# Kernel tuning notes

Hardware: AMD Instinct MI355X
Metric: run time of the kernel (lower is better)

Reference implementation:

```python
import jax, jax.numpy as jnp
import numpy as np

B, C, T = 8, 512, 4096          # batch, channels (query/key/value/calc), time
NUM_HEADS = 8
HEAD_DIM = C // NUM_HEADS
EPS = 1e-6


def _rmsnorm(x, g):
    # x: [B, C, T], normalize over channel dim (num_features)
    return x * jax.lax.rsqrt(jnp.mean(x * x, axis=1, keepdims=True) + EPS) * g[None, :, None]


def _conv1x1(x, W, b):
    # pointwise Conv1d: W [out, in], x [B, in, T]
    return jnp.einsum('oc,bct->bot', W, x) + b[None, :, None]


def _feature(x, W, b, g):
    # Conv1d -> RMSNorm -> elu(x)+1
    return jax.nn.elu(_rmsnorm(_conv1x1(x, W, b), g)) + 1.0


def setup_inputs() -> dict:
    key = jax.random.key(0)
    ks = jax.random.split(key, 16)
    s = 1.0 / np.sqrt(C)
    inp = {
        'queries': jax.random.normal(ks[0], (B, C, T), dtype=jnp.float32),
        'keys': jax.random.normal(ks[1], (B, C, T), dtype=jnp.float32),
        'values': jax.random.normal(ks[2], (B, C, T), dtype=jnp.float32),
        'key_padding_masks': jax.random.randint(ks[3], (B, T), 0, 2).astype(bool),
        'Wq': jax.random.normal(ks[4], (C, C), dtype=jnp.float32) * s,
        'bq': jnp.zeros((C,), dtype=jnp.float32),
        'gq': jnp.ones((C,), dtype=jnp.float32),
        'Wk': jax.random.normal(ks[5], (C, C), dtype=jnp.float32) * s,
        'bk': jnp.zeros((C,), dtype=jnp.float32),
        'gk': jnp.ones((C,), dtype=jnp.float32),
        'Wv': jax.random.normal(ks[6], (C, C), dtype=jnp.float32) * s,
        'bv': jnp.zeros((C,), dtype=jnp.float32),
        'gv': jnp.ones((C,), dtype=jnp.float32),
        'Wp': jax.random.normal(ks[7], (C, C), dtype=jnp.float32) * s,
        'bp': jnp.zeros((C,), dtype=jnp.float32),
        'g_out': jnp.ones((C,), dtype=jnp.float32),
    }
    return inp


def reference(queries, keys, values, key_padding_masks,
              Wq, bq, gq, Wk, bk, gk, Wv, bv, gv, Wp, bp, g_out):
    residuals = queries
    q = _feature(queries, Wq, bq, gq)   # [B, C, Tq]
    k = _feature(keys, Wk, bk, gk)      # [B, C, Tk]
    v = _feature(values, Wv, bv, gv)    # [B, C, Tk]

    # split heads: (head dim) channel layout -> [B, H, Dh, T]
    q = q.reshape(B, NUM_HEADS, HEAD_DIM, -1)
    k = k.reshape(B, NUM_HEADS, HEAD_DIM, -1)
    v = v.reshape(B, NUM_HEADS, HEAD_DIM, -1)

    k = jnp.where(key_padding_masks[:, None, None, :], -10000.0, k)

    q = jax.nn.softmax(q, axis=2) * (NUM_HEADS ** -0.5)  # softmax over head_dim
    k = jax.nn.softmax(k, axis=3)                         # softmax over key time
    v = v / HEAD_DIM

    # linear attention: KV composition then QKV
    ctx = jnp.einsum('bhkt,bhvt->bhkv', k, v)             # [B, H, Dh, Dh]
    out = jnp.einsum('bhqt,bhqv->bhvt', q, ctx)           # [B, H, Dh, Tq]

    out = out.reshape(B, C, -1)
    out = _conv1x1(out, Wp, bp)
    return _rmsnorm(out + residuals, g_out)
```

## Files before the change

kernel.cpp:

```cpp
#include <hip/hip_runtime.h>
#include <hip/hip_bf16.h>

#define BB 8
#define CC 512
#define TT 4096
#define HH 8
#define DH 64
#define EPS 1e-6f

#define NROWS (BB * TT)

using bf16x8 = __attribute__((ext_vector_type(8))) short;
using s16x4  = __attribute__((ext_vector_type(4))) short;
using f32x4  = __attribute__((ext_vector_type(4))) float;

__device__ __forceinline__ short f2b(float f) {
  __hip_bfloat16 h = __float2bfloat16(f);
  return *reinterpret_cast<short*>(&h);
}
__device__ __forceinline__ float b2f(short s) {
  unsigned u = ((unsigned)(unsigned short)s) << 16;
  return __uint_as_float(u);
}

__device__ __forceinline__ void gld16(short* lds_dst, const short* gsrc) {
  __builtin_amdgcn_global_load_lds(
      (const __attribute__((address_space(1))) unsigned int*)gsrc,
      (__attribute__((address_space(3))) unsigned int*)lds_dst, 16, 0, 0);
}

__global__ __launch_bounds__(256) void conv_w4(const float* __restrict__ s0, const float* __restrict__ s1,
                                               const float* __restrict__ s2, const float* __restrict__ s3,
                                               short* __restrict__ d0, short* __restrict__ d1,
                                               short* __restrict__ d2, short* __restrict__ d3)
{
  const float* src; short* dst;
  switch (blockIdx.y) {
    case 0: src = s0; dst = d0; break;
    case 1: src = s1; dst = d1; break;
    case 2: src = s2; dst = d2; break;
    default: src = s3; dst = d3; break;
  }
  int i8 = (blockIdx.x * 256 + threadIdx.x) * 8;
  float4 a = *(const float4*)(src + i8);
  float4 b = *(const float4*)(src + i8 + 4);
  bf16x8 h = { f2b(a.x), f2b(a.y), f2b(a.z), f2b(a.w),
               f2b(b.x), f2b(b.y), f2b(b.z), f2b(b.w) };
  *(bf16x8*)(dst + i8) = h;
}

#define TSTR 120
__device__ __forceinline__ int tadr(int c, int t) {
  return c * TSTR + ((c >> 3) & 7) * 8 + t;
}

__global__ __launch_bounds__(256) void transpose_cvt3(const float* __restrict__ X0,
                                                      const float* __restrict__ X1,
                                                      const float* __restrict__ X2,
                                                      short* __restrict__ Y0,
                                                      short* __restrict__ Y1,
                                                      short* __restrict__ Y2)
{
  __shared__ short tile[2][64 * TSTR];
  const int t0 = blockIdx.x * 256, c0 = blockIdx.y * 64;
  const int b = blockIdx.z & 7, which = blockIdx.z >> 3;
  const float* X = which == 0 ? X0 : (which == 1 ? X1 : X2);
  short* Xt = which == 0 ? Y0 : (which == 1 ? Y1 : Y2);
  const int tid = threadIdx.x;
  const int cl = tid >> 4, t4 = (tid & 15) * 4;
  const int T2 = (tid >> 3) * 2, ci = (tid & 7) * 8;

  float4 r[4];
  #pragma unroll
  for (int it = 0; it < 4; ++it)
    r[it] = *(const float4*)(X + ((size_t)b * CC + c0 + it * 16 + cl) * TT + t0 + t4);

  for (int s = 0; s < 4; ++s) {
    const int cur = s & 1;
    #pragma unroll
    for (int it = 0; it < 4; ++it) {
      s16x4 h = { f2b(r[it].x), f2b(r[it].y), f2b(r[it].z), f2b(r[it].w) };
      *(s16x4*)&tile[cur][tadr(it * 16 + cl, t4)] = h;
    }
    if (s < 3) {
      #pragma unroll
      for (int it = 0; it < 4; ++it)
        r[it] = *(const float4*)(X + ((size_t)b * CC + c0 + it * 16 + cl) * TT
                                 + t0 + (s + 1) * 64 + t4);
    }
    __syncthreads();
    unsigned u[8];
    #pragma unroll
    for (int i = 0; i < 8; ++i)
      u[i] = *(const unsigned*)&tile[cur][tadr(ci + i, T2)];
    short lo[8], hi[8];
    #pragma unroll
    for (int i = 0; i < 8; ++i) {
      lo[i] = (short)(u[i] & 0xffffu);
      hi[i] = (short)(u[i] >> 16);
    }
    short* dst0 = Xt + ((size_t)b * TT + t0 + s * 64 + T2) * CC + c0 + ci;
    *(bf16x8*)dst0 = *(bf16x8*)&lo[0];
    *(bf16x8*)(dst0 + CC) = *(bf16x8*)&hi[0];
  }
}

__device__ __forceinline__ void gemm_body(const short* __restrict__ A,
                                          const short* __restrict__ W,
                                          const float* __restrict__ bias,
                                          short* __restrict__ Y,
                                          short* As, short* Bs, int x, int tid)
{
  int wg = (x & 7) * 128 + (x >> 3);
  const int m0 = (wg >> 2) * 128;
  const int o0 = (wg & 3) * 128;

  const int wid = tid >> 6, lane = tid & 63;
  const int wr = (wid >> 1) * 64, wc = (wid & 1) * 64;
  const int lr = lane & 15, g = lane >> 4;
  const int swz8 = (g ^ ((lr >> 1) & 3)) * 8;

  const int srow0 = tid >> 2;
  const int scol  = ((tid & 3) ^ ((tid >> 3) & 3)) * 8;

  f32x4 acc[4][4] = {};

  #pragma unroll
  for (int it = 0; it < 2; ++it) {
    int row = it * 64 + srow0;
    gld16(&As[it * 2048 + tid * 8], A + (size_t)(m0 + row) * CC + scol);
    gld16(&Bs[it * 2048 + tid * 8], W + (size_t)(o0 + row) * CC + scol);
  }
  __syncthreads();

  for (int step = 0; step < 16; ++step) {
    const int cur = step & 1;
    if (step < 15) {
      const int k0 = (step + 1) * 32;
      #pragma unroll
      for (int it = 0; it < 2; ++it) {
        int row = it * 64 + srow0;
        gld16(&As[(cur ^ 1) * 4096 + it * 2048 + tid * 8], A + (size_t)(m0 + row) * CC + k0 + scol);
        gld16(&Bs[(cur ^ 1) * 4096 + it * 2048 + tid * 8], W + (size_t)(o0 + row) * CC + k0 + scol);
      }
    }
    bf16x8 af[4], bf[4];
    #pragma unroll
    for (int m = 0; m < 4; ++m) af[m] = *(const bf16x8*)&As[cur * 4096 + (wr + m * 16 + lr) * 32 + swz8];
    #pragma unroll
    for (int n = 0; n < 4; ++n) bf[n] = *(const bf16x8*)&Bs[cur * 4096 + (wc + n * 16 + lr) * 32 + swz8];
    #pragma unroll
    for (int m = 0; m < 4; ++m)
      #pragma unroll
      for (int n = 0; n < 4; ++n)
        acc[m][n] = __builtin_amdgcn_mfma_f32_16x16x32_bf16(af[m], bf[n], acc[m][n], 0, 0, 0);
    __syncthreads();
  }

  const int lq4 = (lane >> 4) * 4;
  #pragma unroll
  for (int m = 0; m < 4; ++m)
    #pragma unroll
    for (int r = 0; r < 4; ++r) {
      size_t row = (size_t)(m0 + wr + m * 16 + lq4 + r) * CC;
      #pragma unroll
      for (int n = 0; n < 4; ++n) {
        int o = o0 + wc + n * 16 + lr;
        Y[row + o] = f2b(acc[m][n][r] + bias[o]);
      }
    }
}

__global__ __launch_bounds__(256) void gemm_tc3(
    const short* __restrict__ A0, const short* __restrict__ A1, const short* __restrict__ A2,
    const short* __restrict__ W0, const short* __restrict__ W1, const short* __restrict__ W2,
    const float* __restrict__ b0, const float* __restrict__ b1, const float* __restrict__ b2,
    short* __restrict__ Y0, short* __restrict__ Y1, short* __restrict__ Y2)
{
  __shared__ short As[2 * 4096];
  __shared__ short Bs[2 * 4096];
  const short *A, *W; const float* bias; short* Y;
  switch (blockIdx.y) {
    case 0:  A = A0; W = W0; bias = b0; Y = Y0; break;
    case 1:  A = A1; W = W1; bias = b1; Y = Y1; break;
    default: A = A2; W = W2; bias = b2; Y = Y2; break;
  }
  gemm_body(A, W, bias, Y, As, Bs, blockIdx.x, threadIdx.x);
}

__global__ __launch_bounds__(256) void gemm_tc(const short* __restrict__ A,
                                               const short* __restrict__ W,
                                               const float* __restrict__ bias,
                                               short* __restrict__ Y)
{
  __shared__ short As[2 * 4096];
  __shared__ short Bs[2 * 4096];
  gemm_body(A, W, bias, Y, As, Bs, blockIdx.x, threadIdx.x);
}

__global__ __launch_bounds__(256) void feat_all(short* __restrict__ qf, short* __restrict__ kf,
                                                short* __restrict__ vf,
                                                const float* __restrict__ gq,
                                                const float* __restrict__ gk,
                                                const float* __restrict__ gv,
                                                const unsigned char* __restrict__ mask)
{
  const int mode = blockIdx.y;
  short* buf = mode == 0 ? qf : (mode == 1 ? kf : vf);
  const float* g = mode == 0 ? gq : (mode == 1 ? gk : gv);
  const int row = blockIdx.x * 4 + (threadIdx.x >> 6);
  const int lane = threadIdx.x & 63;
  short* p = buf + (size_t)row * CC + lane * 8;
  if (mode == 1 && mask[row]) {
    bf16x8 z = { 0,0,0,0,0,0,0,0 };
    *(bf16x8*)p = z;
    return;
  }
  bf16x8 v = *(const bf16x8*)p;
  float x[8], ss = 0.f;
  #pragma unroll
  for (int j = 0; j < 8; ++j) { x[j] = b2f(v[j]); ss += x[j] * x[j]; }
  #pragma unroll
  for (int off = 32; off; off >>= 1) ss += __shfl_xor(ss, off);
  float rn = rsqrtf(ss * (1.0f / CC) + EPS);
  float4 g0 = *(const float4*)(g + lane * 8);
  float4 g1 = *(const float4*)(g + lane * 8 + 4);
  float gv8[8] = { g0.x, g0.y, g0.z, g0.w, g1.x, g1.y, g1.z, g1.w };
  float f[8];
  #pragma unroll
  for (int j = 0; j < 8; ++j) {
    float t = x[j] * rn * gv8[j];
    f[j] = t > 0.f ? t + 1.f : __expf(t);
  }
  bf16x8 o;
  if (mode == 1) {
    #pragma unroll
    for (int j = 0; j < 8; ++j) o[j] = f2b(__expf(f[j]));
  } else if (mode == 2) {
    #pragma unroll
    for (int j = 0; j < 8; ++j) o[j] = f2b(f[j] * (1.0f / DH));
  } else {
    float ls = 0.f;
    #pragma unroll
    for (int j = 0; j < 8; ++j) { f[j] = __expf(f[j]); ls += f[j]; }
    ls += __shfl_xor(ls, 1); ls += __shfl_xor(ls, 2); ls += __shfl_xor(ls, 4);
    float sc = 0.35355339059327373f / ls;
    #pragma unroll
    for (int j = 0; j < 8; ++j) o[j] = f2b(f[j] * sc);
  }
  *(bf16x8*)p = o;
}

__global__ __launch_bounds__(256) void ksm_sum(const short* __restrict__ kfe,
                                               float* __restrict__ S)
{
  const int b = blockIdx.y, tch = blockIdx.x;
  const int c2 = threadIdx.x * 2;
  float s0 = 0.f, s1 = 0.f;
  for (int t = 0; t < 128; ++t) {
    unsigned u = *(const unsigned*)&kfe[((size_t)b * TT + tch * 128 + t) * CC + c2];
    s0 += __uint_as_float(u << 16);
    s1 += __uint_as_float(u & 0xffff0000u);
  }
  atomicAdd(&S[b * CC + c2], s0);
  atomicAdd(&S[b * CC + c2 + 1], s1);
}

__global__ __launch_bounds__(256) void ctx_t(const short* __restrict__ kf,
                                             const short* __restrict__ vf,
                                             float* __restrict__ P)
{
  __shared__ short Ks[64 * 64];
  __shared__ short Vs[64 * 64];
  const int tc = blockIdx.x, bh = blockIdx.y;
  const int b = bh >> 3, h = bh & 7;
  const int tid = threadIdx.x, wid = tid >> 6, lane = tid & 63;
  const int lr = lane & 15, lg = lane >> 4;
  f32x4 acc[4] = {};

  for (int ts = 0; ts < 8; ++ts) {
    #pragma unroll
    for (int i = 0; i < 2; ++i) {
      int n = i * 256 + tid;
      int t = n >> 3, ch = (n & 7) * 8;
      size_t src = ((size_t)b * TT + tc * 512 + ts * 64 + t) * CC + h * DH + ch;
      gld16(Ks + n * 8, kf + src);
      gld16(Vs + n * 8, vf + src);
    }
    __syncthreads();
    #pragma unroll
    for (int kk = 0; kk < 64; kk += 32) {
      short a[8];
      #pragma unroll
      for (int j = 0; j < 8; ++j)
        a[j] = Ks[(kk + lg * 8 + j) * 64 + wid * 16 + lr];
      bf16x8 af = *(const bf16x8*)&a[0];
      #pragma unroll
      for (int n = 0; n < 4; ++n) {
        short bv[8];
        #pragma unroll
        for (int j = 0; j < 8; ++j)
          bv[j] = Vs[(kk + lg * 8 + j) * 64 + n * 16 + lr];
        acc[n] = __builtin_amdgcn_mfma_f32_16x16x32_bf16(af, *(const bf16x8*)&bv[0],
                                                         acc[n], 0, 0, 0);
      }
    }
    __syncthreads();
  }
  float* pp = P + ((size_t)tc * 64 + bh) * (DH * DH);
  const int lq4 = lg * 4;
  #pragma unroll
  for (int n = 0; n < 4; ++n)
    #pragma unroll
    for (int r = 0; r < 4; ++r)
      pp[(wid * 16 + lq4 + r) * DH + n * 16 + lr] = acc[n][r];
}

__global__ __launch_bounds__(256) void ctx_reduce(const float* __restrict__ P,
                                                  const float* __restrict__ S,
                                                  short* __restrict__ CT)
{
  int i = blockIdx.x * 256 + threadIdx.x;
  float s = 0.f;
  #pragma unroll
  for (int c = 0; c < 8; ++c) s += P[(size_t)c * 64 * DH * DH + i];
  int bh = i >> 12, rem = i & 4095, q = rem >> 6, v = rem & 63;
  int b = bh >> 3, h = bh & 7;
  float inv = 1.f / S[b * CC + h * DH + q];
  CT[((size_t)bh << 12) + v * 64 + q] = f2b(s * inv);
}

__global__ __launch_bounds__(256) void attn_t(const short* __restrict__ qf,
                                              const short* __restrict__ CT,
                                              short* __restrict__ ao)
{
  __shared__ short As[128 * 72];
  __shared__ short Cs[64 * 72];
  const int m0 = blockIdx.x * 128, h = blockIdx.y;
  const int tid = threadIdx.x, wid = tid >> 6, lane = tid & 63;
  const int lr = lane & 15, lk8 = (lane >> 4) * 8;

  #pragma unroll
  for (int i = 0; i < 4; ++i) {
    int n = i * 256 + tid;
    int r = n >> 3, ch = (n & 7) * 8;
    *(bf16x8*)&As[r * 72 + ch] =
        *(const bf16x8*)(qf + (size_t)(m0 + r) * CC + h * DH + ch);
  }
  {
    const int bh0 = (m0 / TT) * 8 + h;
    #pragma unroll
    for (int i = 0; i < 2; ++i) {
      int n = i * 256 + tid;
      int v = n >> 3, ch = (n & 7) * 8;
      *(bf16x8*)&Cs[v * 72 + ch] = *(const bf16x8*)(CT + ((size_t)bh0 << 12) + v * 64 + ch);
    }
  }
  __syncthreads();

  const int wr = wid * 32;
  f32x4 acc[2][4] = {};
  #pragma unroll
  for (int kk = 0; kk < 64; kk += 32) {
    bf16x8 af[2], cf[4];
    #pragma unroll
    for (int m = 0; m < 2; ++m) af[m] = *(const bf16x8*)&As[(wr + m * 16 + lr) * 72 + kk + lk8];
    #pragma unroll
    for (int n = 0; n < 4; ++n) cf[n] = *(const bf16x8*)&Cs[(n * 16 + lr) * 72 + kk + lk8];
    #pragma unroll
    for (int m = 0; m < 2; ++m)
      #pragma unroll
      for (int n = 0; n < 4; ++n)
        acc[m][n] = __builtin_amdgcn_mfma_f32_16x16x32_bf16(af[m], cf[n], acc[m][n], 0, 0, 0);
  }
  const int lq4 = (lane >> 4) * 4;
  #pragma unroll
  for (int m = 0; m < 2; ++m)
    #pragma unroll
    for (int r = 0; r < 4; ++r) {
      size_t row = (size_t)(m0 + wr + m * 16 + lq4 + r) * CC + h * DH;
      #pragma unroll
      for (int n = 0; n < 4; ++n)
        ao[row + n * 16 + lr] = f2b(acc[m][n][r]);
    }
}

__global__ __launch_bounds__(256) void final_fused(const short* __restrict__ pj,
                                                   const short* __restrict__ qt,
                                                   const float* __restrict__ g,
                                                   float* __restrict__ out)
{
  __shared__ short z[512 * 72];
  __shared__ float rmss[64];
  const int t0 = blockIdx.x * 64, b = blockIdx.y;
  const int tid = threadIdx.x;

  {
    const int t = tid >> 2, cb = (tid & 3) * 128;
    const size_t row = ((size_t)b * TT + t0 + t) * CC + cb;
    float ss = 0.f;
    #pragma unroll
    for (int j = 0; j < 16; ++j) {
      bf16x8 a = *(const bf16x8*)(pj + row + j * 8);
      bf16x8 q = *(const bf16x8*)(qt + row + j * 8);
      #pragma unroll
      for (int e = 0; e < 8; ++e) {
        float zf = b2f(a[e]) + b2f(q[e]);
        ss += zf * zf;
        z[(cb + j * 8 + e) * 72 + t] = f2b(zf);
      }
    }
    ss += __shfl_xor(ss, 1);
    ss += __shfl_xor(ss, 2);
    if ((tid & 3) == 0) rmss[t] = rsqrtf(ss * (1.0f / CC) + EPS);
  }
  __syncthreads();

  const int c = tid >> 2, tcs = (tid & 3) * 16;
  #pragma unroll 1
  for (int cb8 = 0; cb8 < 8; ++cb8) {
    const int cc = cb8 * 64 + c;
    const float gc = g[cc];
    bf16x8 z0 = *(const bf16x8*)&z[cc * 72 + tcs];
    bf16x8 z1 = *(const bf16x8*)&z[cc * 72 + tcs + 8];
    float* dst = out + ((size_t)b * CC + cc) * TT + t0 + tcs;
    #pragma unroll
    for (int i = 0; i < 2; ++i) {
      float4 o0 = { b2f(z0[i*4+0]) * rmss[tcs+i*4+0] * gc, b2f(z0[i*4+1]) * rmss[tcs+i*4+1] * gc,
                    b2f(z0[i*4+2]) * rmss[tcs+i*4+2] * gc, b2f(z0[i*4+3]) * rmss[tcs+i*4+3] * gc };
      *(float4*)(dst + i * 4) = o0;
    }
    #pragma unroll
    for (int i = 0; i < 2; ++i) {
      float4 o1 = { b2f(z1[i*4+0]) * rmss[tcs+8+i*4+0] * gc, b2f(z1[i*4+1]) * rmss[tcs+8+i*4+1] * gc,
                    b2f(z1[i*4+2]) * rmss[tcs+8+i*4+2] * gc, b2f(z1[i*4+3]) * rmss[tcs+8+i*4+3] * gc };
      *(float4*)(dst + 8 + i * 4) = o1;
    }
  }
}

extern "C" void kernel_launch(void* const* d_in, const int* in_sizes, int n_in,
                              void* d_out, int out_size, void* d_ws, size_t ws_size,
                              hipStream_t stream) {
  (void)in_sizes; (void)n_in; (void)out_size; (void)ws_size;
  const float* queries = (const float*)d_in[0];
  const float* keys    = (const float*)d_in[1];
  const float* values  = (const float*)d_in[2];
  const unsigned char* mask = (const unsigned char*)d_in[3];
  const float* Wq = (const float*)d_in[4];
  const float* bq = (const float*)d_in[5];
  const float* gq = (const float*)d_in[6];
  const float* Wk = (const float*)d_in[7];
  const float* bk = (const float*)d_in[8];
  const float* gk = (const float*)d_in[9];
  const float* Wv = (const float*)d_in[10];
  const float* bv = (const float*)d_in[11];
  const float* gv = (const float*)d_in[12];
  const float* Wp = (const float*)d_in[13];
  const float* bp = (const float*)d_in[14];
  const float* g_out = (const float*)d_in[15];

  const size_t NCT = (size_t)NROWS * CC;
  short* qt = (short*)d_ws;
  short* kt = qt + NCT;
  short* vt = kt + NCT;
  short* qf = vt + NCT;
  short* kf = qf + NCT;
  short* vf = kf + NCT;
  short* ao = kt;
  short* pj = vt;
  float* ctxP = (float*)(vf + NCT);
  short* CT  = (short*)(ctxP + (size_t)8 * 64 * DH * DH);
  short* wqb = CT + (size_t)64 * DH * DH;
  short* wkb = wqb + (size_t)CC * CC;
  short* wvb = wkb + (size_t)CC * CC;
  short* wpb = wvb + (size_t)CC * CC;
  float* S   = (float*)(wpb + (size_t)CC * CC);

  hipMemsetAsync(S, 0, (size_t)BB * CC * sizeof(float), stream);

  conv_w4<<<dim3(CC * CC / 2048, 4), 256, 0, stream>>>(Wq, Wk, Wv, Wp, wqb, wkb, wvb, wpb);

  transpose_cvt3<<<dim3(TT / 256, CC / 64, 3 * BB), 256, 0, stream>>>(
      queries, keys, values, qt, kt, vt);

  gemm_tc3<<<dim3(1024, 3), 256, 0, stream>>>(qt, kt, vt, wqb, wkb, wvb,
                                              bq, bk, bv, qf, kf, vf);

  feat_all<<<dim3(NROWS / 4, 3), 256, 0, stream>>>(qf, kf, vf, gq, gk, gv, mask);

  ksm_sum<<<dim3(32, BB), 256, 0, stream>>>(kf, S);

  ctx_t<<<dim3(8, BB * HH), 256, 0, stream>>>(kf, vf, ctxP);
  ctx_reduce<<<dim3(64 * DH * DH / 256), 256, 0, stream>>>(ctxP, S, CT);

  attn_t<<<dim3(NROWS / 128, HH), 256, 0, stream>>>(qf, CT, ao);

  gemm_tc<<<dim3(1024), 256, 0, stream>>>(ao, wpb, bp, pj);

  final_fused<<<dim3(TT / 64, BB), 256, 0, stream>>>(pj, qt, g_out, (float*)d_out);
}
```

Before: 315.4 us.

## Replace syncthreads with fine-grained vmcnt waits and raw barriers in transpose and GEMM

The GEMM main loop now waits with s_waitcnt vmcnt(4) before its barrier, so the next tile's async global-to-LDS loads can stay in flight while the current tile is consumed. Previously __syncthreads drained every outstanding load. The transpose kernel drops its double-buffered LDS tile for a single buffer, prefetches the next chunk into registers before writing the current one, and uses raw s_barrier plus sched_barrier fences. This is meant to cut LDS use and stall time, at the risk of subtle races if the vmcnt counts or barrier placement are wrong.

```diff
diff --git a/kernel.cpp b/kernel.cpp
--- a/kernel.cpp
+++ b/kernel.cpp
@@ -61,7 +61,7 @@
                                                       short* __restrict__ Y1,
                                                       short* __restrict__ Y2)
 {
-  __shared__ short tile[2][64 * TSTR];
+  __shared__ short tile[64 * TSTR];
   const int t0 = blockIdx.x * 256, c0 = blockIdx.y * 64;
   const int b = blockIdx.z & 7, which = blockIdx.z >> 3;
   const float* X = which == 0 ? X0 : (which == 1 ? X1 : X2);
@@ -70,29 +70,32 @@
   const int cl = tid >> 4, t4 = (tid & 15) * 4;
   const int T2 = (tid >> 3) * 2, ci = (tid & 7) * 8;
 
-  float4 r[4];
+  float4 rc[4];
   #pragma unroll
   for (int it = 0; it < 4; ++it)
-    r[it] = *(const float4*)(X + ((size_t)b * CC + c0 + it * 16 + cl) * TT + t0 + t4);
-
+    rc[it] = *(const float4*)(X + ((size_t)b * CC + c0 + it * 16 + cl) * TT + t0 + t4);
+
+  #pragma unroll
   for (int s = 0; s < 4; ++s) {
-    const int cur = s & 1;
+    float4 rn[4];
+    if (s < 3) {
+      #pragma unroll
+      for (int it = 0; it < 4; ++it)
+        rn[it] = *(const float4*)(X + ((size_t)b * CC + c0 + it * 16 + cl) * TT
+                                  + t0 + (s + 1) * 64 + t4);
+    }
     #pragma unroll
     for (int it = 0; it < 4; ++it) {
-      s16x4 h = { f2b(r[it].x), f2b(r[it].y), f2b(r[it].z), f2b(r[it].w) };
-      *(s16x4*)&tile[cur][tadr(it * 16 + cl, t4)] = h;
-    }
-    if (s < 3) {
-      #pragma unroll
-      for (int it = 0; it < 4; ++it)
-        r[it] = *(const float4*)(X + ((size_t)b * CC + c0 + it * 16 + cl) * TT
-                                 + t0 + (s + 1) * 64 + t4);
-    }
-    __syncthreads();
+      s16x4 h = { f2b(rc[it].x), f2b(rc[it].y), f2b(rc[it].z), f2b(rc[it].w) };
+      *(s16x4*)&tile[tadr(it * 16 + cl, t4)] = h;
+    }
+    asm volatile("s_waitcnt lgkmcnt(0)" ::: "memory");
+    __builtin_amdgcn_s_barrier();
+    __builtin_amdgcn_sched_barrier(0);
     unsigned u[8];
     #pragma unroll
     for (int i = 0; i < 8; ++i)
-      u[i] = *(const unsigned*)&tile[cur][tadr(ci + i, T2)];
+      u[i] = *(const unsigned*)&tile[tadr(ci + i, T2)];
     short lo[8], hi[8];
     #pragma unroll
     for (int i = 0; i < 8; ++i) {
@@ -102,6 +105,11 @@
     short* dst0 = Xt + ((size_t)b * TT + t0 + s * 64 + T2) * CC + c0 + ci;
     *(bf16x8*)dst0 = *(bf16x8*)&lo[0];
     *(bf16x8*)(dst0 + CC) = *(bf16x8*)&hi[0];
+    __builtin_amdgcn_sched_barrier(0);
+    __builtin_amdgcn_s_barrier();
+    __builtin_amdgcn_sched_barrier(0);
+    #pragma unroll
+    for (int it = 0; it < 4; ++it) rc[it] = rn[it];
   }
 }
 
@@ -131,7 +139,6 @@
     gld16(&As[it * 2048 + tid * 8], A + (size_t)(m0 + row) * CC + scol);
     gld16(&Bs[it * 2048 + tid * 8], W + (size_t)(o0 + row) * CC + scol);
   }
-  __syncthreads();
 
   for (int step = 0; step < 16; ++step) {
     const int cur = step & 1;
@@ -143,7 +150,13 @@
         gld16(&As[(cur ^ 1) * 4096 + it * 2048 + tid * 8], A + (size_t)(m0 + row) * CC + k0 + scol);
         gld16(&Bs[(cur ^ 1) * 4096 + it * 2048 + tid * 8], W + (size_t)(o0 + row) * CC + k0 + scol);
       }
-    }
+      asm volatile("s_waitcnt vmcnt(4)" ::: "memory");
+    } else {
+      asm volatile("s_waitcnt vmcnt(0)" ::: "memory");
+    }
+    __builtin_amdgcn_s_barrier();
+    __builtin_amdgcn_sched_barrier(0);
+
     bf16x8 af[4], bf[4];
     #pragma unroll
     for (int m = 0; m < 4; ++m) af[m] = *(const bf16x8*)&As[cur * 4096 + (wr + m * 16 + lr) * 32 + swz8];
@@ -154,7 +167,10 @@
       #pragma unroll
       for (int n = 0; n < 4; ++n)
         acc[m][n] = __builtin_amdgcn_mfma_f32_16x16x32_bf16(af[m], bf[n], acc[m][n], 0, 0, 0);
-    __syncthreads();
+
+    __builtin_amdgcn_sched_barrier(0);
+    __builtin_amdgcn_s_barrier();
+    __builtin_amdgcn_sched_barrier(0);
   }
 
   const int lq4 = (lane >> 4) * 4;
```

Result: no change. 320.6 us (+1.7%).

## Fuse per-head attention output with output projection GEMM in one kernel

Applied to the files above, without the earlier changes.

Replaces the separate attn_t kernel and the projection GEMM with a single kernel. For each head, the kernel computes the Q·ctx tile into shared memory and immediately accumulates it against the matching slice of Wp. This removes the round trip of the ao intermediate through global memory and one launch. In exchange, each 128x128 output tile recomputes the Q·ctx product for all 8 heads, so 4 column tiles repeat it, and the loop has per-head syncs and no double buffering.

```diff
diff --git a/kernel.cpp b/kernel.cpp
--- a/kernel.cpp
+++ b/kernel.cpp
@@ -185,16 +185,6 @@
     case 1:  A = A1; W = W1; bias = b1; Y = Y1; break;
     default: A = A2; W = W2; bias = b2; Y = Y2; break;
   }
-  gemm_body(A, W, bias, Y, As, Bs, blockIdx.x, threadIdx.x);
-}
-
-__global__ __launch_bounds__(256) void gemm_tc(const short* __restrict__ A,
-                                               const short* __restrict__ W,
-                                               const float* __restrict__ bias,
-                                               short* __restrict__ Y)
-{
-  __shared__ short As[2 * 4096];
-  __shared__ short Bs[2 * 4096];
   gemm_body(A, W, bias, Y, As, Bs, blockIdx.x, threadIdx.x);
 }
 
@@ -330,58 +320,100 @@
   CT[((size_t)bh << 12) + v * 64 + q] = f2b(s * inv);
 }
 
-__global__ __launch_bounds__(256) void attn_t(const short* __restrict__ qf,
-                                              const short* __restrict__ CT,
-                                              short* __restrict__ ao)
-{
-  __shared__ short As[128 * 72];
+__global__ __launch_bounds__(256) void attn_proj(const short* __restrict__ qf,
+                                                 const short* __restrict__ CT,
+                                                 const short* __restrict__ Wp,
+                                                 const float* __restrict__ bp,
+                                                 short* __restrict__ pj)
+{
+  __shared__ short Qs[128 * 72];
   __shared__ short Cs[64 * 72];
-  const int m0 = blockIdx.x * 128, h = blockIdx.y;
-  const int tid = threadIdx.x, wid = tid >> 6, lane = tid & 63;
-  const int lr = lane & 15, lk8 = (lane >> 4) * 8;
-
-  #pragma unroll
-  for (int i = 0; i < 4; ++i) {
-    int n = i * 256 + tid;
-    int r = n >> 3, ch = (n & 7) * 8;
-    *(bf16x8*)&As[r * 72 + ch] =
-        *(const bf16x8*)(qf + (size_t)(m0 + r) * CC + h * DH + ch);
-  }
-  {
-    const int bh0 = (m0 / TT) * 8 + h;
+  __shared__ short Ws2[128 * 72];
+  __shared__ short AOs[128 * 72];
+  const int tid = threadIdx.x;
+  int x = blockIdx.x;
+  int wg = (x & 7) * 128 + (x >> 3);
+  const int m0 = (wg >> 2) * 128;
+  const int o0 = (wg & 3) * 128;
+  const int wid = tid >> 6, lane = tid & 63;
+  const int lr = lane & 15, lg = lane >> 4, lk8 = lg * 8;
+  const int wr = (wid >> 1) * 64, wc = (wid & 1) * 64;
+  const int bh0 = (m0 >> 12) * 8;
+
+  f32x4 acc[4][4] = {};
+
+  for (int h = 0; h < 8; ++h) {
+    #pragma unroll
+    for (int i = 0; i < 4; ++i) {
+      int n = i * 256 + tid;
+      int r = n >> 3, ch = (n & 7) * 8;
+      *(bf16x8*)&Qs[r * 72 + ch]  = *(const bf16x8*)(qf + (size_t)(m0 + r) * CC + h * DH + ch);
+      *(bf16x8*)&Ws2[r * 72 + ch] = *(const bf16x8*)(Wp + (size_t)(o0 + r) * CC + h * DH + ch);
+    }
     #pragma unroll
     for (int i = 0; i < 2; ++i) {
       int n = i * 256 + tid;
       int v = n >> 3, ch = (n & 7) * 8;
-      *(bf16x8*)&Cs[v * 72 + ch] = *(const bf16x8*)(CT + ((size_t)bh0 << 12) + v * 64 + ch);
-    }
-  }
-  __syncthreads();
-
-  const int wr = wid * 32;
-  f32x4 acc[2][4] = {};
-  #pragma unroll
-  for (int kk = 0; kk < 64; kk += 32) {
-    bf16x8 af[2], cf[4];
-    #pragma unroll
-    for (int m = 0; m < 2; ++m) af[m] = *(const bf16x8*)&As[(wr + m * 16 + lr) * 72 + kk + lk8];
-    #pragma unroll
-    for (int n = 0; n < 4; ++n) cf[n] = *(const bf16x8*)&Cs[(n * 16 + lr) * 72 + kk + lk8];
-    #pragma unroll
-    for (int m = 0; m < 2; ++m)
-      #pragma unroll
-      for (int n = 0; n < 4; ++n)
-        acc[m][n] = __builtin_amdgcn_mfma_f32_16x16x32_bf16(af[m], cf[n], acc[m][n], 0, 0, 0);
-  }
-  const int lq4 = (lane >> 4) * 4;
-  #pragma unroll
-  for (int m = 0; m < 2; ++m)
+      *(bf16x8*)&Cs[v * 72 + ch] = *(const bf16x8*)(CT + ((size_t)(bh0 + h) << 12) + v * 64 + ch);
+    }
+    __syncthreads();
+
+    f32x4 aoacc[2][4] = {};
+    #pragma unroll
+    for (int ks = 0; ks < 2; ++ks) {
+      bf16x8 afq[2], cfv[4];
+      #pragma unroll
+      for (int mf = 0; mf < 2; ++mf)
+        afq[mf] = *(const bf16x8*)&Qs[(wid * 32 + mf * 16 + lr) * 72 + ks * 32 + lk8];
+      #pragma unroll
+      for (int nf = 0; nf < 4; ++nf)
+        cfv[nf] = *(const bf16x8*)&Cs[(nf * 16 + lr) * 72 + ks * 32 + lk8];
+      #pragma unroll
+      for (int mf = 0; mf < 2; ++mf)
+        #pragma unroll
+        for (int nf = 0; nf < 4; ++nf)
+          aoacc[mf][nf] = __builtin_amdgcn_mfma_f32_16x16x32_bf16(afq[mf], cfv[nf], aoacc[mf][nf], 0, 0, 0);
+    }
+    #pragma unroll
+    for (int mf = 0; mf < 2; ++mf)
+      #pragma unroll
+      for (int r = 0; r < 4; ++r) {
+        int row = wid * 32 + mf * 16 + lg * 4 + r;
+        #pragma unroll
+        for (int nf = 0; nf < 4; ++nf)
+          AOs[row * 72 + nf * 16 + lr] = f2b(aoacc[mf][nf][r]);
+      }
+    __syncthreads();
+
+    #pragma unroll
+    for (int ks = 0; ks < 2; ++ks) {
+      bf16x8 afa[4], bfw[4];
+      #pragma unroll
+      for (int mf = 0; mf < 4; ++mf)
+        afa[mf] = *(const bf16x8*)&AOs[(wr + mf * 16 + lr) * 72 + ks * 32 + lk8];
+      #pragma unroll
+      for (int nf = 0; nf < 4; ++nf)
+        bfw[nf] = *(const bf16x8*)&Ws2[(wc + nf * 16 + lr) * 72 + ks * 32 + lk8];
+      #pragma unroll
+      for (int mf = 0; mf < 4; ++mf)
+        #pragma unroll
+        for (int nf = 0; nf < 4; ++nf)
+          acc[mf][nf] = __builtin_amdgcn_mfma_f32_16x16x32_bf16(afa[mf], bfw[nf], acc[mf][nf], 0, 0, 0);
+    }
+    __syncthreads();
+  }
+
+  const int lq4 = lg * 4;
+  #pragma unroll
+  for (int mf = 0; mf < 4; ++mf)
     #pragma unroll
     for (int r = 0; r < 4; ++r) {
-      size_t row = (size_t)(m0 + wr + m * 16 + lq4 + r) * CC + h * DH;
-      #pragma unroll
-      for (int n = 0; n < 4; ++n)
-        ao[row + n * 16 + lr] = f2b(acc[m][n][r]);
+      size_t row = (size_t)(m0 + wr + mf * 16 + lq4 + r) * CC;
+      #pragma unroll
+      for (int nf = 0; nf < 4; ++nf) {
+        int o = o0 + wc + nf * 16 + lr;
+        pj[row + o] = f2b(acc[mf][nf][r] + bp[o]);
+      }
     }
 }
 
@@ -467,7 +499,6 @@
   short* qf = vt + NCT;
   short* kf = qf + NCT;
   short* vf = kf + NCT;
-  short* ao = kt;
   short* pj = vt;
   float* ctxP = (float*)(vf + NCT);
   short* CT  = (short*)(ctxP + (size_t)8 * 64 * DH * DH);
@@ -494,9 +525,7 @@
   ctx_t<<<dim3(8, BB * HH), 256, 0, stream>>>(kf, vf, ctxP);
   ctx_reduce<<<dim3(64 * DH * DH / 256), 256, 0, stream>>>(ctxP, S, CT);
 
-  attn_t<<<dim3(NROWS / 128, HH), 256, 0, stream>>>(qf, CT, ao);
-
-  gemm_tc<<<dim3(1024), 256, 0, stream>>>(ao, wpb, bp, pj);
+  attn_proj<<<dim3(1024), 256, 0, stream>>>(qf, CT, wpb, bp, pj);
 
   final_fused<<<dim3(TT / 64, BB), 256, 0, stream>>>(pj, qt, g_out, (float*)d_out);
 }
```

Result: slower. 323.4 us (+2.5%).

## Fuse fp32-to-bf16 transpose into GEMM for key and value projections

Applied to the files above, without the earlier changes.

Keys and values no longer go through a separate transpose-and-convert pass to bf16 [B*T, C] buffers. A new GEMM kernel reads the fp32 [B, C, T] input directly, converts it to bf16 and transposes it into a swizzled LDS tile while prefetching the next K-slice in registers. Queries still use the old transpose path because the transposed bf16 copy is needed later as the residual. This removes one full write and re-read of two activation tensors, at the cost of fp32 global loads inside the GEMM main loop and extra LDS staging work per step.

```diff
diff --git a/kernel.cpp b/kernel.cpp
--- a/kernel.cpp
+++ b/kernel.cpp
@@ -54,18 +54,11 @@
   return c * TSTR + ((c >> 3) & 7) * 8 + t;
 }
 
-__global__ __launch_bounds__(256) void transpose_cvt3(const float* __restrict__ X0,
-                                                      const float* __restrict__ X1,
-                                                      const float* __restrict__ X2,
-                                                      short* __restrict__ Y0,
-                                                      short* __restrict__ Y1,
-                                                      short* __restrict__ Y2)
+__global__ __launch_bounds__(256) void transpose_cvt1(const float* __restrict__ X,
+                                                      short* __restrict__ Xt)
 {
   __shared__ short tile[2][64 * TSTR];
-  const int t0 = blockIdx.x * 256, c0 = blockIdx.y * 64;
-  const int b = blockIdx.z & 7, which = blockIdx.z >> 3;
-  const float* X = which == 0 ? X0 : (which == 1 ? X1 : X2);
-  short* Xt = which == 0 ? Y0 : (which == 1 ? Y1 : Y2);
+  const int t0 = blockIdx.x * 256, c0 = blockIdx.y * 64, b = blockIdx.z;
   const int tid = threadIdx.x;
   const int cl = tid >> 4, t4 = (tid & 15) * 4;
   const int T2 = (tid >> 3) * 2, ci = (tid & 7) * 8;
@@ -105,12 +98,15 @@
   }
 }
 
-__device__ __forceinline__ void gemm_body(const short* __restrict__ A,
-                                          const short* __restrict__ W,
-                                          const float* __restrict__ bias,
-                                          short* __restrict__ Y,
-                                          short* As, short* Bs, int x, int tid)
-{
+__global__ __launch_bounds__(256) void gemm_tc(const short* __restrict__ A,
+                                               const short* __restrict__ W,
+                                               const float* __restrict__ bias,
+                                               short* __restrict__ Y)
+{
+  __shared__ short As[2 * 4096];
+  __shared__ short Bs[2 * 4096];
+  const int tid = threadIdx.x;
+  int x = blockIdx.x;
   int wg = (x & 7) * 128 + (x >> 3);
   const int m0 = (wg >> 2) * 128;
   const int o0 = (wg & 3) * 128;
@@ -119,7 +115,6 @@
   const int wr = (wid >> 1) * 64, wc = (wid & 1) * 64;
   const int lr = lane & 15, g = lane >> 4;
   const int swz8 = (g ^ ((lr >> 1) & 3)) * 8;
-
   const int srow0 = tid >> 2;
   const int scol  = ((tid & 3) ^ ((tid >> 3) & 3)) * 8;
 
@@ -171,31 +166,101 @@
     }
 }
 
-__global__ __launch_bounds__(256) void gemm_tc3(
-    const short* __restrict__ A0, const short* __restrict__ A1, const short* __restrict__ A2,
-    const short* __restrict__ W0, const short* __restrict__ W1, const short* __restrict__ W2,
-    const float* __restrict__ b0, const float* __restrict__ b1, const float* __restrict__ b2,
-    short* __restrict__ Y0, short* __restrict__ Y1, short* __restrict__ Y2)
-{
-  __shared__ short As[2 * 4096];
-  __shared__ short Bs[2 * 4096];
-  const short *A, *W; const float* bias; short* Y;
-  switch (blockIdx.y) {
-    case 0:  A = A0; W = W0; bias = b0; Y = Y0; break;
-    case 1:  A = A1; W = W1; bias = b1; Y = Y1; break;
-    default: A = A2; W = W2; bias = b2; Y = Y2; break;
-  }
-  gemm_body(A, W, bias, Y, As, Bs, blockIdx.x, threadIdx.x);
-}
-
-__global__ __launch_bounds__(256) void gemm_tc(const short* __restrict__ A,
-                                               const short* __restrict__ W,
-                                               const float* __restrict__ bias,
-                                               short* __restrict__ Y)
-{
-  __shared__ short As[2 * 4096];
-  __shared__ short Bs[2 * 4096];
-  gemm_body(A, W, bias, Y, As, Bs, blockIdx.x, threadIdx.x);
+#define AST 40
+__device__ __forceinline__ int aadr(int m, int c) {
+  return m * AST + ((m >> 2) & 7) * 8 + c;
+}
+
+__global__ __launch_bounds__(256) void gemm_direct2(
+    const float* __restrict__ X0, const float* __restrict__ X1,
+    const short* __restrict__ W0, const short* __restrict__ W1,
+    const float* __restrict__ b0, const float* __restrict__ b1,
+    short* __restrict__ Y0, short* __restrict__ Y1)
+{
+  __shared__ short Am[2][5184];
+  __shared__ short Ws[2][4096];
+  const float* Xf = blockIdx.y == 0 ? X0 : X1;
+  const short* W  = blockIdx.y == 0 ? W0 : W1;
+  const float* bias = blockIdx.y == 0 ? b0 : b1;
+  short* Y        = blockIdx.y == 0 ? Y0 : Y1;
+
+  const int tid = threadIdx.x;
+  int x = blockIdx.x;
+  int wg = (x & 7) * 128 + (x >> 3);
+  const int m0 = (wg >> 2) * 128;
+  const int o0 = (wg & 3) * 128;
+  const int b = m0 >> 12, t0 = m0 & 4095;
+  const float* Xb = Xf + (size_t)b * CC * TT + t0;
+
+  const int wid = tid >> 6, lane = tid & 63;
+  const int wr = (wid >> 1) * 64, wc = (wid & 1) * 64;
+  const int lr = lane & 15, g = lane >> 4;
+  const int lk8 = g * 8;
+  const int swz8 = (g ^ ((lr >> 1) & 3)) * 8;
+  const int srow0 = tid >> 2;
+  const int scol  = ((tid & 3) ^ ((tid >> 3) & 3)) * 8;
+
+  const int t4 = (tid & 31) * 4;
+  const int c4 = (tid >> 5) * 4;
+
+  f32x4 acc[4][4] = {};
+
+  float4 rc[4];
+  #pragma unroll
+  for (int j = 0; j < 4; ++j)
+    rc[j] = *(const float4*)(Xb + (size_t)(c4 + j) * TT + t4);
+  #pragma unroll
+  for (int it = 0; it < 2; ++it)
+    gld16(&Ws[0][it * 2048 + tid * 8], W + (size_t)(o0 + it * 64 + srow0) * CC + scol);
+
+  for (int step = 0; step < 16; ++step) {
+    const int cur = step & 1;
+    float4 rn[4];
+    if (step < 15) {
+      const int k0 = (step + 1) * 32;
+      #pragma unroll
+      for (int j = 0; j < 4; ++j)
+        rn[j] = *(const float4*)(Xb + (size_t)(k0 + c4 + j) * TT + t4);
+      #pragma unroll
+      for (int it = 0; it < 2; ++it)
+        gld16(&Ws[cur ^ 1][it * 2048 + tid * 8], W + (size_t)(o0 + it * 64 + srow0) * CC + k0 + scol);
+    }
+    #pragma unroll
+    for (int jt = 0; jt < 4; ++jt) {
+      int m = t4 + jt;
+      s16x4 h = { f2b(rc[0][jt]), f2b(rc[1][jt]), f2b(rc[2][jt]), f2b(rc[3][jt]) };
+      *(s16x4*)&Am[cur][aadr(m, c4)] = h;
+    }
+    __syncthreads();
+
+    bf16x8 af[4], bf[4];
+    #pragma unroll
+    for (int m = 0; m < 4; ++m) af[m] = *(const bf16x8*)&Am[cur][aadr(wr + m * 16 + lr, lk8)];
+    #pragma unroll
+    for (int n = 0; n < 4; ++n) bf[n] = *(const bf16x8*)&Ws[cur][(wc + n * 16 + lr) * 32 + swz8];
+    #pragma unroll
+    for (int m = 0; m < 4; ++m)
+      #pragma unroll
+      for (int n = 0; n < 4; ++n)
+        acc[m][n] = __builtin_amdgcn_mfma_f32_16x16x32_bf16(af[m], bf[n], acc[m][n], 0, 0, 0);
+    __syncthreads();
+
+    #pragma unroll
+    for (int j = 0; j < 4; ++j) rc[j] = rn[j];
+  }
+
+  const int lq4 = (lane >> 4) * 4;
+  #pragma unroll
+  for (int m = 0; m < 4; ++m)
+    #pragma unroll
+    for (int r = 0; r < 4; ++r) {
+      size_t row = (size_t)(m0 + wr + m * 16 + lq4 + r) * CC;
+      #pragma unroll
+      for (int n = 0; n < 4; ++n) {
+        int o = o0 + wc + n * 16 + lr;
+        Y[row + o] = f2b(acc[m][n][r] + bias[o]);
+      }
+    }
 }
 
 __global__ __launch_bounds__(256) void feat_all(short* __restrict__ qf, short* __restrict__ kf,
@@ -462,14 +527,12 @@
 
   const size_t NCT = (size_t)NROWS * CC;
   short* qt = (short*)d_ws;
-  short* kt = qt + NCT;
-  short* vt = kt + NCT;
-  short* qf = vt + NCT;
+  short* qf = qt + NCT;
   short* kf = qf + NCT;
   short* vf = kf + NCT;
-  short* ao = kt;
-  short* pj = vt;
-  float* ctxP = (float*)(vf + NCT);
+  short* ao = vf + NCT;
+  short* pj = ao + NCT;
+  float* ctxP = (float*)(pj + NCT);
   short* CT  = (short*)(ctxP + (size_t)8 * 64 * DH * DH);
   short* wqb = CT + (size_t)64 * DH * DH;
   short* wkb = wqb + (size_t)CC * CC;
@@ -481,11 +544,12 @@
 
   conv_w4<<<dim3(CC * CC / 2048, 4), 256, 0, stream>>>(Wq, Wk, Wv, Wp, wqb, wkb, wvb, wpb);
 
-  transpose_cvt3<<<dim3(TT / 256, CC / 64, 3 * BB), 256, 0, stream>>>(
-      queries, keys, values, qt, kt, vt);
-
-  gemm_tc3<<<dim3(1024, 3), 256, 0, stream>>>(qt, kt, vt, wqb, wkb, wvb,
-                                              bq, bk, bv, qf, kf, vf);
+  transpose_cvt1<<<dim3(TT / 256, CC / 64, BB), 256, 0, stream>>>(queries, qt);
+
+  gemm_tc<<<dim3(1024), 256, 0, stream>>>(qt, wqb, bq, qf);
+
+  gemm_direct2<<<dim3(1024, 2), 256, 0, stream>>>(keys, values, wkb, wvb,
+                                                  bk, bv, kf, vf);
 
   feat_all<<<dim3(NROWS / 4, 3), 256, 0, stream>>>(qf, kf, vf, gq, gk, gv, mask);
 
```

Measured after the change: 298.5 us. 1.06x faster.
